# Kernel tuning notes

Hardware: AMD Instinct MI355X
Metric: run time of the kernel (lower is better)

Reference implementation:

```python
import jax, jax.numpy as jnp
import numpy as np

N = 512
C = 64
B = 1048576


def setup_inputs() -> dict:
    key = jax.random.key(0)
    k1, k2, k3, k4 = jax.random.split(key, 4)
    coords = jax.random.uniform(k1, (B, 3), dtype=jnp.float32, minval=-0.5, maxval=0.5)
    x_line = jax.random.normal(k2, (N, C), dtype=jnp.float32)
    y_line = jax.random.normal(k3, (N, C), dtype=jnp.float32)
    z_line = jax.random.normal(k4, (N, C), dtype=jnp.float32)
    grid = jnp.linspace(-0.5, 0.5, N, dtype=jnp.float32)
    return {"coords": coords, "x_line": x_line, "y_line": y_line, "z_line": z_line, "grid": grid}


def _interp_1d(line_feat, coord, grid):
    # line_feat: [N, C], coord: [B] in [-0.5, 0.5]
    n = line_feat.shape[0]
    pos = (coord - grid[0]) / (grid[1] - grid[0])          # [B] fractional index
    idx0 = jnp.clip(jnp.floor(pos).astype(jnp.int32), 0, n - 2)
    w1 = (pos - idx0.astype(pos.dtype))[:, None]            # [B, 1]
    f0 = line_feat[idx0]                                    # [B, C] gather
    f1 = line_feat[idx0 + 1]                                # [B, C] gather
    return f0 * (1.0 - w1) + f1 * w1


def reference(coords, x_line, y_line, z_line, grid):
    # mode='sum' (default): fx + fy + fz -> [B, C]
    fx = _interp_1d(x_line, coords[:, 0], grid)
    fy = _interp_1d(y_line, coords[:, 1], grid)
    fz = _interp_1d(z_line, coords[:, 2], grid)
    return fx + fy + fz
```

## Files before the change

### kernel.cpp

```cpp
#include <hip/hip_runtime.h>


typedef float f4 __attribute__((ext_vector_type(4)));

constexpr int kN  = 512;
constexpr int kC4 = 16;

__global__ __launch_bounds__(256) void triline_kernel(
    const float* __restrict__ coords,
    const f4* __restrict__ xl,
    const f4* __restrict__ yl,
    const f4* __restrict__ zl,
    const float* __restrict__ grid,
    f4* __restrict__ out,
    int total)
{
    int gid = blockIdx.x * 256 + threadIdx.x;
    if (gid >= total) return;
    int b  = gid >> 4;
    int c4 = gid & 15;

    float g0     = grid[0];
    float inv_dg = 1.0f / (grid[1] - g0);

    float cx = coords[3 * b + 0];
    float cy = coords[3 * b + 1];
    float cz = coords[3 * b + 2];

    float px = (cx - g0) * inv_dg;
    float py = (cy - g0) * inv_dg;
    float pz = (cz - g0) * inv_dg;

    int ix = min(max((int)floorf(px), 0), kN - 2);
    int iy = min(max((int)floorf(py), 0), kN - 2);
    int iz = min(max((int)floorf(pz), 0), kN - 2);

    float wx = px - (float)ix;
    float wy = py - (float)iy;
    float wz = pz - (float)iz;

    f4 x0 = xl[ix * kC4 + c4];
    f4 x1 = xl[ix * kC4 + kC4 + c4];
    f4 y0 = yl[iy * kC4 + c4];
    f4 y1 = yl[iy * kC4 + kC4 + c4];
    f4 z0 = zl[iz * kC4 + c4];
    f4 z1 = zl[iz * kC4 + kC4 + c4];

    f4 r = x0 + (x1 - x0) * wx;
    r    = r + y0 + (y1 - y0) * wy;
    r    = r + z0 + (z1 - z0) * wz;

    __builtin_nontemporal_store(r, &out[gid]);
}

extern "C" void kernel_launch(void* const* d_in, const int* in_sizes, int n_in,
                              void* d_out, int out_size, void* d_ws, size_t ws_size,
                              hipStream_t stream) {
    const float* coords = (const float*)d_in[0];
    const f4*    xl     = (const f4*)d_in[1];
    const f4*    yl     = (const f4*)d_in[2];
    const f4*    zl     = (const f4*)d_in[3];
    const float* grid   = (const float*)d_in[4];
    f4*          out    = (f4*)d_out;

    int B      = in_sizes[0] / 3;
    int total  = B * kC4;
    int blocks = (total + 255) / 256;

    triline_kernel<<<blocks, 256, 0, stream>>>(coords, xl, yl, zl, grid, out, total);
}
```

Before: 334.0 us.

## Stage channel-sliced line tables in LDS with persistent blocks

Each block copies one 16-channel slice of all three line tables (padded rows) into LDS. It then walks a contiguous range of points in a persistent grid-stride loop and prefetches the next point's coords. The gathers now hit LDS instead of global memory or L2, and the padding is meant to reduce bank conflicts. In exchange, coords are read once per channel group and each point's output is written as scattered 64-byte pieces rather than full rows. The roughly 120KB LDS footprint limits each CU to one block.

```diff
diff --git a/kernel.cpp b/kernel.cpp
--- a/kernel.cpp
+++ b/kernel.cpp
@@ -3,54 +3,98 @@
 
 typedef float f4 __attribute__((ext_vector_type(4)));
 
-constexpr int kN  = 512;
-constexpr int kC4 = 16;
+constexpr int kN       = 512;
+constexpr int kC4      = 16;
+constexpr int kGroups  = 4;
+constexpr int kPr      = 128;
+constexpr int kRowF    = 20;
+constexpr int kThreads = 1024;
 
-__global__ __launch_bounds__(256) void triline_kernel(
+__global__ __launch_bounds__(kThreads) void triline_lds_kernel(
     const float* __restrict__ coords,
     const f4* __restrict__ xl,
     const f4* __restrict__ yl,
     const f4* __restrict__ zl,
     const float* __restrict__ grid,
     f4* __restrict__ out,
-    int total)
+    int B)
 {
-    int gid = blockIdx.x * 256 + threadIdx.x;
-    if (gid >= total) return;
-    int b  = gid >> 4;
-    int c4 = gid & 15;
+    __shared__ float sm[3 * kN * kRowF];
 
-    float g0     = grid[0];
-    float inv_dg = 1.0f / (grid[1] - g0);
+    const int bid = blockIdx.x;
+    const int g   = bid / kPr;
+    const int pr  = bid % kPr;
 
-    float cx = coords[3 * b + 0];
-    float cy = coords[3 * b + 1];
-    float cz = coords[3 * b + 2];
+    for (int i = threadIdx.x; i < kN * 4; i += kThreads) {
+        const int r   = i >> 2;
+        const int k   = i & 3;
+        const int dst = r * kRowF + k * 4;
+        const int src = r * kC4 + g * 4 + k;
+        *(f4*)&sm[dst]                  = xl[src];
+        *(f4*)&sm[kN * kRowF + dst]     = yl[src];
+        *(f4*)&sm[2 * kN * kRowF + dst] = zl[src];
+    }
+    __syncthreads();
 
-    float px = (cx - g0) * inv_dg;
-    float py = (cy - g0) * inv_dg;
-    float pz = (cz - g0) * inv_dg;
+    const float g0     = grid[0];
+    const float inv_dg = 1.0f / (grid[1] - g0);
 
-    int ix = min(max((int)floorf(px), 0), kN - 2);
-    int iy = min(max((int)floorf(py), 0), kN - 2);
-    int iz = min(max((int)floorf(pz), 0), kN - 2);
+    const int p = threadIdx.x >> 2;
+    const int k = threadIdx.x & 3;
 
-    float wx = px - (float)ix;
-    float wy = py - (float)iy;
-    float wz = pz - (float)iz;
+    const int per  = (B + kPr - 1) / kPr;
+    const int b0   = pr * per;
+    const int bend = min(b0 + per, B);
 
-    f4 x0 = xl[ix * kC4 + c4];
-    f4 x1 = xl[ix * kC4 + kC4 + c4];
-    f4 y0 = yl[iy * kC4 + c4];
-    f4 y1 = yl[iy * kC4 + kC4 + c4];
-    f4 z0 = zl[iz * kC4 + c4];
-    f4 z1 = zl[iz * kC4 + kC4 + c4];
+    const float* sx = sm;
+    const float* sy = sm + kN * kRowF;
+    const float* sz = sm + 2 * kN * kRowF;
 
-    f4 r = x0 + (x1 - x0) * wx;
-    r    = r + y0 + (y1 - y0) * wy;
-    r    = r + z0 + (z1 - z0) * wz;
+    int   b  = b0 + p;
+    float cx = 0.0f, cy = 0.0f, cz = 0.0f;
+    if (b < bend) {
+        cx = coords[3 * b + 0];
+        cy = coords[3 * b + 1];
+        cz = coords[3 * b + 2];
+    }
 
-    __builtin_nontemporal_store(r, &out[gid]);
+    while (b < bend) {
+        const int bn = b + 256;
+        float nx = 0.0f, ny = 0.0f, nz = 0.0f;
+        if (bn < bend) {
+            nx = coords[3 * bn + 0];
+            ny = coords[3 * bn + 1];
+            nz = coords[3 * bn + 2];
+        }
+
+        const float px = (cx - g0) * inv_dg;
+        const float py = (cy - g0) * inv_dg;
+        const float pz = (cz - g0) * inv_dg;
+
+        const int ix = min(max((int)floorf(px), 0), kN - 2);
+        const int iy = min(max((int)floorf(py), 0), kN - 2);
+        const int iz = min(max((int)floorf(pz), 0), kN - 2);
+
+        const float wx = px - (float)ix;
+        const float wy = py - (float)iy;
+        const float wz = pz - (float)iz;
+
+        const f4 x0 = *(const f4*)&sx[ix * kRowF + k * 4];
+        const f4 x1 = *(const f4*)&sx[ix * kRowF + kRowF + k * 4];
+        const f4 y0 = *(const f4*)&sy[iy * kRowF + k * 4];
+        const f4 y1 = *(const f4*)&sy[iy * kRowF + kRowF + k * 4];
+        const f4 z0 = *(const f4*)&sz[iz * kRowF + k * 4];
+        const f4 z1 = *(const f4*)&sz[iz * kRowF + kRowF + k * 4];
+
+        f4 r = x0 + (x1 - x0) * wx;
+        r    = r + y0 + (y1 - y0) * wy;
+        r    = r + z0 + (z1 - z0) * wz;
+
+        __builtin_nontemporal_store(r, &out[b * kC4 + g * 4 + k]);
+
+        b  = bn;
+        cx = nx; cy = ny; cz = nz;
+    }
 }
 
 extern "C" void kernel_launch(void* const* d_in, const int* in_sizes, int n_in,
@@ -63,9 +107,8 @@
     const float* grid   = (const float*)d_in[4];
     f4*          out    = (f4*)d_out;
 
-    int B      = in_sizes[0] / 3;
-    int total  = B * kC4;
-    int blocks = (total + 255) / 256;
+    int B = in_sizes[0] / 3;
 
-    triline_kernel<<<blocks, 256, 0, stream>>>(coords, xl, yl, zl, grid, out, total);
+    triline_lds_kernel<<<kGroups * kPr, kThreads, 0, stream>>>(
+        coords, xl, yl, zl, grid, out, B);
 }
```

Result: faster. 318.0 us (-4.8%).
